# Kernel optimization log

Hardware: AMD Instinct MI355X
Metric: run time of the kernel (lower is better)

The kernel has to match this reference:

```python
import jax, jax.numpy as jnp
import numpy as np

B, S, D = 8, 512, 1024
F = 4 * D        # FFN hidden
E = 8            # num experts
SCALE = 0.02


def setup_inputs() -> dict:
    key = jax.random.key(0)
    ks = jax.random.split(key, 16)
    n = lambda k, shape, s=SCALE: (jax.random.normal(k, shape, dtype=jnp.float32) * s)
    task_ids = jax.random.randint(ks[15], (B,), 0, E)
    return {
        "hidden_states": jax.random.normal(ks[0], (B, S, D), dtype=jnp.float32),
        "ohe_task": jax.nn.one_hot(task_ids, E, dtype=jnp.float32),
        # base model (2-layer FFN) params
        "W1": n(ks[1], (D, F)), "b1": n(ks[2], (F,)),
        "W2": n(ks[3], (F, D)), "b2": n(ks[4], (D,)),
        # expert task vectors (expert_sd - base_sd), stacked over experts
        "T_W1": n(ks[5], (E, D, F)), "T_b1": n(ks[6], (E, F)),
        "T_W2": n(ks[7], (E, F, D)), "T_b2": n(ks[8], (E, D)),
        # gate: 2 hidden ReLU layers then linear to E
        "Wg1": n(ks[9], (D, D)), "bg1": jnp.zeros((D,), jnp.float32),
        "Wg2": n(ks[10], (D, D)), "bg2": jnp.zeros((D,), jnp.float32),
        "Wgo": n(ks[11], (D, E)), "bgo": jnp.zeros((E,), jnp.float32),
    }


def reference(hidden_states, ohe_task, W1, b1, W2, b2,
              T_W1, T_b1, T_W2, T_b2,
              Wg1, bg1, Wg2, bg2, Wgo, bgo):
    x = hidden_states  # [B,S,D]
    # --- router: per-token logits -> softmax over experts -> mean over seq ---
    h = jax.nn.relu(jnp.einsum("bsd,de->bse", x, Wg1) + bg1)
    h = jax.nn.relu(jnp.einsum("bsd,de->bse", h, Wg2) + bg2)
    logits = jnp.einsum("bsd,de->bse", h, Wgo) + bgo        # [B,S,E]
    gate_weights = jax.nn.softmax(logits, axis=-1).mean(axis=1)  # [B,E]
    # --- per-sample weighted merge of expert task vectors into base params ---
    coeff = gate_weights + ohe_task                          # [B,E]
    W1b = W1 + jnp.einsum("be,edf->bdf", coeff, T_W1)        # [B,D,F]
    b1b = b1 + coeff @ T_b1                                  # [B,F]
    W2b = W2 + jnp.einsum("be,efd->bfd", coeff, T_W2)        # [B,F,D]
    b2b = b2 + coeff @ T_b2                                  # [B,D]
    # --- batched functional forward through merged FFN ---
    hmid = jax.nn.gelu(jnp.einsum("bsd,bdf->bsf", x, W1b) + b1b[:, None, :],
                       approximate=False)
    out = jnp.einsum("bsf,bfd->bsd", hmid, W2b) + b2b[:, None, :]
    return out, gate_weights
```

## Files before the change

kernel.cpp:

```cpp
#include <hip/hip_runtime.h>
#include <hip/hip_bf16.h>

typedef __attribute__((ext_vector_type(8))) short s16x8;
typedef __attribute__((ext_vector_type(4))) float f32x4;

#define GLOAD_LDS16(gsrc, ldst) \
  __builtin_amdgcn_global_load_lds((const __attribute__((address_space(1))) void*)(gsrc), \
      (__attribute__((address_space(3))) void*)(ldst), 16, 0, 0)

__global__ __launch_bounds__(256) void cvt_bf16(const float* __restrict__ in,
                                                __hip_bfloat16* __restrict__ out, long n) {
  long i = ((long)blockIdx.x * 256 + threadIdx.x) * 4;
  if (i + 3 >= n) return;
  float4 v = *(const float4*)(in + i);
  __hip_bfloat16 tmp[4] = {__float2bfloat16(v.x), __float2bfloat16(v.y),
                           __float2bfloat16(v.z), __float2bfloat16(v.w)};
  *(ushort4*)((unsigned short*)out + i) = *(const ushort4*)tmp;
}

template<int NB>
__global__ __launch_bounds__(256) void merge_transpose(
    const float* __restrict__ Wb, const float* __restrict__ T,
    const float* __restrict__ coeff, __hip_bfloat16* __restrict__ Out,
    int K, int N, int nE) {
  int ntn = N >> 6;
  int k0 = (blockIdx.x / ntn) << 6;
  int n0 = (blockIdx.x % ntn) << 6;
  int t = threadIdx.x;
  long KN = (long)K * N;

  float4 accb[NB][4];
#pragma unroll
  for (int i = 0; i < 4; ++i) {
    int e = i * 256 + t; int kk = e >> 4, nn = (e & 15) << 2;
    float4 bv = *(const float4*)&Wb[(long)(k0 + kk) * N + n0 + nn];
#pragma unroll
    for (int b2 = 0; b2 < NB; ++b2) accb[b2][i] = bv;
  }
  for (int ex = 0; ex < nE; ++ex) {
    float c[NB];
#pragma unroll
    for (int b2 = 0; b2 < NB; ++b2) c[b2] = coeff[b2 * 8 + ex];
#pragma unroll
    for (int i = 0; i < 4; ++i) {
      int e = i * 256 + t; int kk = e >> 4, nn = (e & 15) << 2;
      float4 tv = *(const float4*)&T[(long)ex * KN + (long)(k0 + kk) * N + n0 + nn];
#pragma unroll
      for (int b2 = 0; b2 < NB; ++b2) {
        accb[b2][i].x += c[b2] * tv.x; accb[b2][i].y += c[b2] * tv.y;
        accb[b2][i].z += c[b2] * tv.z; accb[b2][i].w += c[b2] * tv.w;
      }
    }
  }
  __shared__ __hip_bfloat16 lds[64 * 66];
  for (int b2 = 0; b2 < NB; ++b2) {
    __syncthreads();
#pragma unroll
    for (int i = 0; i < 4; ++i) {
      int e = i * 256 + t; int kk = e >> 4, nn = (e & 15) << 2;
      lds[kk * 66 + nn + 0] = __float2bfloat16(accb[b2][i].x);
      lds[kk * 66 + nn + 1] = __float2bfloat16(accb[b2][i].y);
      lds[kk * 66 + nn + 2] = __float2bfloat16(accb[b2][i].z);
      lds[kk * 66 + nn + 3] = __float2bfloat16(accb[b2][i].w);
    }
    __syncthreads();
#pragma unroll
    for (int i = 0; i < 4; ++i) {
      int o = i * 256 + t; int n2 = o >> 4, k2 = (o & 15) << 2;
      __hip_bfloat16 tmp[4];
#pragma unroll
      for (int j = 0; j < 4; ++j) tmp[j] = lds[(k2 + j) * 66 + n2];
      *(ushort4*)((unsigned short*)&Out[(long)b2 * KN + (long)(n0 + n2) * K + k0 + k2]) =
          *(const ushort4*)tmp;
    }
  }
}

__global__ __launch_bounds__(256) void merge_bias(const float* __restrict__ base,
                                                  const float* __restrict__ T,
                                                  const float* __restrict__ coeff,
                                                  float* __restrict__ out, int n) {
  int b = blockIdx.y;
  int i = blockIdx.x * 256 + threadIdx.x;
  if (i >= n) return;
  float v = base[i];
#pragma unroll
  for (int e = 0; e < 8; ++e) v += coeff[b * 8 + e] * T[(long)e * n + i];
  out[(long)b * n + i] = v;
}

template<int MODE, int ACT, bool OUTBF>
__global__ __launch_bounds__(256, 2) void gemm_bt(
    const __hip_bfloat16* __restrict__ A, const __hip_bfloat16* __restrict__ BT,
    const float* __restrict__ bias, void* __restrict__ Out,
    int N, int K, long sA, long sB, long sBias, long sOut,
    int kLen, long ksOut) {
  int bid = blockIdx.x;
  int b, m, n, kc = 0;
  if (MODE == 0)      { b = blockIdx.y; m = (bid & 7) * 4 + ((bid >> 3) & 3); n = bid >> 5; }
  else                { b = bid & 7; int tile = bid >> 3; m = tile & 3; n = (tile >> 2) & 7; kc = tile >> 5; }
  int m0 = m << 7, n0 = n << 7;
  int kOff = kc * kLen;

  const __hip_bfloat16* Ab = A + (long)b * sA;
  const __hip_bfloat16* Bb = BT + (long)b * sB;

  __shared__ __align__(16) __hip_bfloat16 As[128 * 64];
  __shared__ __align__(16) __hip_bfloat16 Bs[128 * 64];

  int t = threadIdx.x;
  int lane = t & 63;
  int wid = t >> 6;
  int wm = wid >> 1, wn = wid & 1;
  int lr = lane & 15, kg = lane >> 4;

  f32x4 acc[4][4] = {};

  for (int kt = kOff; kt < kOff + kLen; kt += 64) {
#pragma unroll
    for (int is = 0; is < 4; ++is) {
      int ci = is * 256 + t;
      int row = ci >> 3, cpos = ci & 7;
      int csrc = cpos ^ (row & 7);
      GLOAD_LDS16(Ab + (long)(m0 + row) * K + kt + csrc * 8, &As[ci * 8]);
      GLOAD_LDS16(Bb + (long)(n0 + row) * K + kt + csrc * 8, &Bs[ci * 8]);
    }
    __syncthreads();
#pragma unroll
    for (int ks = 0; ks < 2; ++ks) {
      s16x8 af[4], bfr[4];
#pragma unroll
      for (int mi = 0; mi < 4; ++mi) {
        int row = wm * 64 + mi * 16 + lr;
        int c = (ks * 4 + kg) ^ (row & 7);
        af[mi] = *(const s16x8*)&As[row * 64 + c * 8];
      }
#pragma unroll
      for (int ni = 0; ni < 4; ++ni) {
        int row = wn * 64 + ni * 16 + lr;
        int c = (ks * 4 + kg) ^ (row & 7);
        bfr[ni] = *(const s16x8*)&Bs[row * 64 + c * 8];
      }
#pragma unroll
      for (int mi = 0; mi < 4; ++mi)
#pragma unroll
        for (int ni = 0; ni < 4; ++ni)
          acc[mi][ni] = __builtin_amdgcn_mfma_f32_16x16x32_bf16(bfr[ni], af[mi], acc[mi][ni], 0, 0, 0);
    }
    __syncthreads();
  }

#pragma unroll
  for (int mi = 0; mi < 4; ++mi) {
    int row = m0 + wm * 64 + mi * 16 + lr;
#pragma unroll
    for (int ni = 0; ni < 4; ++ni) {
      int colb = n0 + wn * 64 + ni * 16 + kg * 4;
      float bv4[4] = {0.f, 0.f, 0.f, 0.f};
      if (bias != nullptr) {
        float4 bb = *(const float4*)&bias[(long)b * sBias + colb];
        bv4[0] = bb.x; bv4[1] = bb.y; bv4[2] = bb.z; bv4[3] = bb.w;
      }
      float v[4];
#pragma unroll
      for (int j = 0; j < 4; ++j) {
        v[j] = acc[mi][ni][j] + bv4[j];
        if (ACT == 1) v[j] = fmaxf(v[j], 0.f);
        else if (ACT == 2) v[j] = 0.5f * v[j] * (1.f + erff(v[j] * 0.70710678118f));
      }
      long off = kc * ksOut + (long)b * sOut + (long)row * N + colb;
      if (OUTBF) {
        __hip_bfloat16 tmp[4] = {__float2bfloat16(v[0]), __float2bfloat16(v[1]),
                                 __float2bfloat16(v[2]), __float2bfloat16(v[3])};
        *(ushort4*)((unsigned short*)Out + off) = *(const ushort4*)tmp;
      } else {
        *(float4*)((float*)Out + off) = make_float4(v[0], v[1], v[2], v[3]);
      }
    }
  }
}

__global__ __launch_bounds__(512, 4) void gemm_l1(
    const __hip_bfloat16* __restrict__ A, const __hip_bfloat16* __restrict__ BT,
    const float* __restrict__ bias, __hip_bfloat16* __restrict__ Out) {
  const int K = 1024, N = 4096;
  int bid = blockIdx.x;
  int b = bid & 7;
  int tile = bid >> 3;
  int m0 = (tile & 3) << 7;
  int n0 = (tile >> 2) << 8;

  const __hip_bfloat16* Ab = A + (long)b * 512 * 1024;
  const __hip_bfloat16* Bb = BT + (long)b * 4096 * 1024;
  const float* biasb = bias + (long)b * 4096;

  __shared__ __align__(16) __hip_bfloat16 As[128 * 64];
  __shared__ __align__(16) __hip_bfloat16 Bs[256 * 64];

  int t = threadIdx.x;
  int lane = t & 63;
  int wid = t >> 6;
  int wm = wid >> 2;
  int wn = wid & 3;
  int lr = lane & 15, kg = lane >> 4;

  f32x4 acc[4][4] = {};

  for (int kt = 0; kt < K; kt += 64) {
#pragma unroll
    for (int is = 0; is < 2; ++is) {
      int ci = is * 512 + t;
      int row = ci >> 3, cpos = ci & 7;
      int csrc = cpos ^ (row & 7);
      GLOAD_LDS16(Ab + (long)(m0 + row) * K + kt + csrc * 8, &As[ci * 8]);
    }
#pragma unroll
    for (int is = 0; is < 4; ++is) {
      int ci = is * 512 + t;
      int row = ci >> 3, cpos = ci & 7;
      int csrc = cpos ^ (row & 7);
      GLOAD_LDS16(Bb + (long)(n0 + row) * K + kt + csrc * 8, &Bs[ci * 8]);
    }
    __syncthreads();
#pragma unroll
    for (int ks = 0; ks < 2; ++ks) {
      s16x8 af[4], bfr[4];
#pragma unroll
      for (int mi = 0; mi < 4; ++mi) {
        int row = wm * 64 + mi * 16 + lr;
        int c = (ks * 4 + kg) ^ (row & 7);
        af[mi] = *(const s16x8*)&As[row * 64 + c * 8];
      }
#pragma unroll
      for (int ni = 0; ni < 4; ++ni) {
        int row = wn * 64 + ni * 16 + lr;
        int c = (ks * 4 + kg) ^ (row & 7);
        bfr[ni] = *(const s16x8*)&Bs[row * 64 + c * 8];
      }
#pragma unroll
      for (int mi = 0; mi < 4; ++mi)
#pragma unroll
        for (int ni = 0; ni < 4; ++ni)
          acc[mi][ni] = __builtin_amdgcn_mfma_f32_16x16x32_bf16(bfr[ni], af[mi], acc[mi][ni], 0, 0, 0);
    }
    __syncthreads();
  }

#pragma unroll
  for (int mi = 0; mi < 4; ++mi) {
    int row = m0 + wm * 64 + mi * 16 + lr;
#pragma unroll
    for (int ni = 0; ni < 4; ++ni) {
      int colb = n0 + wn * 64 + ni * 16 + kg * 4;
      float4 bb = *(const float4*)&biasb[colb];
      float v[4] = {acc[mi][ni][0] + bb.x, acc[mi][ni][1] + bb.y,
                    acc[mi][ni][2] + bb.z, acc[mi][ni][3] + bb.w};
#pragma unroll
      for (int j = 0; j < 4; ++j)
        v[j] = 0.5f * v[j] * (1.f + erff(v[j] * 0.70710678118f));
      long off = (long)b * 512 * 4096 + (long)row * N + colb;
      __hip_bfloat16 tmp[4] = {__float2bfloat16(v[0]), __float2bfloat16(v[1]),
                               __float2bfloat16(v[2]), __float2bfloat16(v[3])};
      *(ushort4*)((unsigned short*)Out + off) = *(const ushort4*)tmp;
    }
  }
}

__global__ __launch_bounds__(256) void reduce2_bias(
    const __hip_bfloat16* __restrict__ p, const float* __restrict__ b2b,
    float* __restrict__ out, long ksOut) {
  long i = ((long)blockIdx.x * 256 + threadIdx.x) * 8;
  const unsigned short* ps = (const unsigned short*)p;
  ushort4 a0 = *(const ushort4*)(ps + i);
  ushort4 a1 = *(const ushort4*)(ps + i + 4);
  ushort4 c0 = *(const ushort4*)(ps + ksOut + i);
  ushort4 c1 = *(const ushort4*)(ps + ksOut + i + 4);
  int d = (int)(i & 1023);
  int b = (int)(i >> 19);
  const float* bp = b2b + (long)b * 1024 + d;
  float o[8];
  unsigned short av[8] = {a0.x, a0.y, a0.z, a0.w, a1.x, a1.y, a1.z, a1.w};
  unsigned short cv[8] = {c0.x, c0.y, c0.z, c0.w, c1.x, c1.y, c1.z, c1.w};
#pragma unroll
  for (int j = 0; j < 8; ++j) {
    __hip_bfloat16 ab = *(__hip_bfloat16*)&av[j], cb = *(__hip_bfloat16*)&cv[j];
    o[j] = __bfloat162float(ab) + __bfloat162float(cb) + bp[j];
  }
  *(float4*)(out + i) = make_float4(o[0], o[1], o[2], o[3]);
  *(float4*)(out + i + 4) = make_float4(o[4], o[5], o[6], o[7]);
}

__global__ __launch_bounds__(256) void router_logits(
    const __hip_bfloat16* __restrict__ Hg2, const float* __restrict__ Wgo,
    const float* __restrict__ bgo, float* __restrict__ probs) {
  int r = blockIdx.x;
  int t = threadIdx.x;
  float acc[8] = {};
#pragma unroll
  for (int j = 0; j < 4; ++j) {
    int k = j * 256 + t;
    float h = __bfloat162float(Hg2[(long)r * 1024 + k]);
    const float4* wp = (const float4*)&Wgo[k * 8];
    float4 w0 = wp[0], w1 = wp[1];
    acc[0] += h * w0.x; acc[1] += h * w0.y; acc[2] += h * w0.z; acc[3] += h * w0.w;
    acc[4] += h * w1.x; acc[5] += h * w1.y; acc[6] += h * w1.z; acc[7] += h * w1.w;
  }
#pragma unroll
  for (int off = 32; off >= 1; off >>= 1)
#pragma unroll
    for (int e = 0; e < 8; ++e) acc[e] += __shfl_down(acc[e], off);
  __shared__ float lds[4][8];
  int wid = t >> 6, lane = t & 63;
  if (lane == 0)
#pragma unroll
    for (int e = 0; e < 8; ++e) lds[wid][e] = acc[e];
  __syncthreads();
  if (t == 0) {
    float lg[8];
#pragma unroll
    for (int e = 0; e < 8; ++e) lg[e] = lds[0][e] + lds[1][e] + lds[2][e] + lds[3][e] + bgo[e];
    float mx = lg[0];
#pragma unroll
    for (int e = 1; e < 8; ++e) mx = fmaxf(mx, lg[e]);
    float s = 0.f;
#pragma unroll
    for (int e = 0; e < 8; ++e) { lg[e] = __expf(lg[e] - mx); s += lg[e]; }
    float inv = 1.f / s;
#pragma unroll
    for (int e = 0; e < 8; ++e) probs[(long)r * 8 + e] = lg[e] * inv;
  }
}

__global__ __launch_bounds__(256) void router_mean(
    const float* __restrict__ probs, const float* __restrict__ ohe,
    float* __restrict__ gate_out, float* __restrict__ coeff) {
  int b = blockIdx.x;
  int t = threadIdx.x;
  int e = t & 7, sg = t >> 3;
  float s = 0.f;
#pragma unroll
  for (int j = 0; j < 16; ++j)
    s += probs[((long)b * 512 + sg + j * 32) * 8 + e];
  __shared__ float lds[256];
  lds[t] = s;
  __syncthreads();
  if (t < 8) {
    float tot = 0.f;
#pragma unroll
    for (int g = 0; g < 32; ++g) tot += lds[g * 8 + t];
    float gw = tot / 512.f;
    gate_out[b * 8 + t] = gw;
    coeff[b * 8 + t] = gw + ohe[b * 8 + t];
  }
}

extern "C" void kernel_launch(void* const* d_in, const int* in_sizes, int n_in,
                              void* d_out, int out_size, void* d_ws, size_t ws_size,
                              hipStream_t stream) {
  const float* x    = (const float*)d_in[0];
  const float* ohe  = (const float*)d_in[1];
  const float* W1   = (const float*)d_in[2];
  const float* b1   = (const float*)d_in[3];
  const float* W2   = (const float*)d_in[4];
  const float* b2   = (const float*)d_in[5];
  const float* T_W1 = (const float*)d_in[6];
  const float* T_b1 = (const float*)d_in[7];
  const float* T_W2 = (const float*)d_in[8];
  const float* T_b2 = (const float*)d_in[9];
  const float* Wg1  = (const float*)d_in[10];
  const float* bg1  = (const float*)d_in[11];
  const float* Wg2  = (const float*)d_in[12];
  const float* bg2  = (const float*)d_in[13];
  const float* Wgo  = (const float*)d_in[14];
  const float* bgo  = (const float*)d_in[15];
  float* out = (float*)d_out;
  float* gate_out = out + (long)8 * 512 * 1024;

  char* w = (char*)d_ws;
  __hip_bfloat16* xb   = (__hip_bfloat16*)(w);
  __hip_bfloat16* Wg1T = (__hip_bfloat16*)(w + 8388608);
  __hip_bfloat16* Wg2T = (__hip_bfloat16*)(w + 10485760);
  __hip_bfloat16* Hg1  = (__hip_bfloat16*)(w + 12582912);
  __hip_bfloat16* Hg2  = (__hip_bfloat16*)(w + 20971520);
  float*          probs= (float*)(w + 29360128);
  float*          coeff= (float*)(w + 29491200);
  float*          b1b  = (float*)(w + 29492224);
  float*          b2b  = (float*)(w + 29623296);
  __hip_bfloat16* hmid = (__hip_bfloat16*)(w + 29656064);
  __hip_bfloat16* Wb   = (__hip_bfloat16*)(w + 63210496);
  __hip_bfloat16* part = (__hip_bfloat16*)(w);

  const long SSD = (long)512 * 1024;
  const long SSF = (long)512 * 4096;

  cvt_bf16<<<4096, 256, 0, stream>>>(x, xb, (long)8 * 512 * 1024);
  merge_transpose<1><<<16 * 16, 256, 0, stream>>>(Wg1, nullptr, nullptr, Wg1T, 1024, 1024, 0);
  merge_transpose<1><<<16 * 16, 256, 0, stream>>>(Wg2, nullptr, nullptr, Wg2T, 1024, 1024, 0);
  gemm_bt<0, 1, true><<<dim3(256, 1), 256, 0, stream>>>(xb, Wg1T, bg1, Hg1,
      1024, 1024, 0, 0, 0, 0, 1024, 0);
  gemm_bt<0, 1, true><<<dim3(256, 1), 256, 0, stream>>>(Hg1, Wg2T, bg2, Hg2,
      1024, 1024, 0, 0, 0, 0, 1024, 0);
  router_logits<<<4096, 256, 0, stream>>>(Hg2, Wgo, bgo, probs);
  router_mean<<<8, 256, 0, stream>>>(probs, ohe, gate_out, coeff);
  merge_bias<<<dim3(16, 8), 256, 0, stream>>>(b1, T_b1, coeff, b1b, 4096);
  merge_bias<<<dim3(4, 8), 256, 0, stream>>>(b2, T_b2, coeff, b2b, 1024);
  merge_transpose<8><<<16 * 64, 256, 0, stream>>>(W1, T_W1, coeff, Wb, 1024, 4096, 8);
  gemm_l1<<<dim3(512, 1), 512, 0, stream>>>(xb, Wb, b1b, hmid);
  merge_transpose<8><<<64 * 16, 256, 0, stream>>>(W2, T_W2, coeff, Wb, 4096, 1024, 8);
  gemm_bt<2, 0, true><<<dim3(512, 1), 256, 0, stream>>>(hmid, Wb, nullptr, part,
      1024, 4096, SSF, (long)4096 * 1024, 0, SSD, 2048, (long)8 * 512 * 1024);
  reduce2_bias<<<2048, 256, 0, stream>>>(part, b2b, out, (long)8 * 512 * 1024);
}
```

Measured before the change: 258.6 us.

## Fuse layer-1 GEMM with W2 merge in one launch and split K four ways

Adds a combined kernel whose first 512 blocks run the layer-1 GEMM while the remaining 2048 blocks merge and transpose the W2 expert weights into a separate workspace buffer. This overlaps memory-bound merge work with the compute-bound GEMM instead of running them back to back. The second GEMM now uses a 4-way K split (1024 blocks) with a generalized partial-sum reduction, which needs a larger workspace. A fallback path keeps the old sequence when the workspace is too small. The W2 merge blocks use a 64x64 tile with per-element LDS stores, and each block processes 4 of the 8 batches at once.

```diff
diff --git a/kernel.cpp b/kernel.cpp
--- a/kernel.cpp
+++ b/kernel.cpp
@@ -180,11 +180,11 @@
   }
 }
 
-__global__ __launch_bounds__(512, 4) void gemm_l1(
+__device__ __forceinline__ void l1_gemm_body(
+    int bid, int t, __hip_bfloat16* As, __hip_bfloat16* Bs,
     const __hip_bfloat16* __restrict__ A, const __hip_bfloat16* __restrict__ BT,
     const float* __restrict__ bias, __hip_bfloat16* __restrict__ Out) {
   const int K = 1024, N = 4096;
-  int bid = blockIdx.x;
   int b = bid & 7;
   int tile = bid >> 3;
   int m0 = (tile & 3) << 7;
@@ -194,10 +194,6 @@
   const __hip_bfloat16* Bb = BT + (long)b * 4096 * 1024;
   const float* biasb = bias + (long)b * 4096;
 
-  __shared__ __align__(16) __hip_bfloat16 As[128 * 64];
-  __shared__ __align__(16) __hip_bfloat16 Bs[256 * 64];
-
-  int t = threadIdx.x;
   int lane = t & 63;
   int wid = t >> 6;
   int wm = wid >> 2;
@@ -266,25 +262,103 @@
   }
 }
 
-__global__ __launch_bounds__(256) void reduce2_bias(
+__global__ __launch_bounds__(512, 4) void gemm_l1(
+    const __hip_bfloat16* __restrict__ A, const __hip_bfloat16* __restrict__ BT,
+    const float* __restrict__ bias, __hip_bfloat16* __restrict__ Out) {
+  __shared__ __align__(16) __hip_bfloat16 As[128 * 64];
+  __shared__ __align__(16) __hip_bfloat16 Bs[256 * 64];
+  l1_gemm_body(blockIdx.x, threadIdx.x, As, Bs, A, BT, bias, Out);
+}
+
+__global__ __launch_bounds__(512, 4) void fused_l1_w2(
+    const __hip_bfloat16* __restrict__ A, const __hip_bfloat16* __restrict__ BT,
+    const float* __restrict__ bias, __hip_bfloat16* __restrict__ Out,
+    const float* __restrict__ W2, const float* __restrict__ T2,
+    const float* __restrict__ coeff, __hip_bfloat16* __restrict__ Out2) {
+  __shared__ __align__(16) char smem[49152];
+  int bid = blockIdx.x;
+  int t = threadIdx.x;
+  if (bid < 512) {
+    __hip_bfloat16* As = (__hip_bfloat16*)smem;
+    __hip_bfloat16* Bs = As + 128 * 64;
+    l1_gemm_body(bid, t, As, Bs, A, BT, bias, Out);
+    return;
+  }
+  __hip_bfloat16* lds = (__hip_bfloat16*)smem;
+  int mid = bid - 512;
+  int q = (mid & 1) * 4;
+  int tileId = mid >> 1;
+  const int K = 4096, N = 1024;
+  int k0 = (tileId >> 4) << 6;
+  int n0 = (tileId & 15) << 6;
+  long KN = (long)K * N;
+
+  float4 accb[4][2];
+#pragma unroll
+  for (int i = 0; i < 2; ++i) {
+    int c = i * 512 + t; int kk = c >> 4, nn = (c & 15) << 2;
+    float4 bv = *(const float4*)&W2[(long)(k0 + kk) * N + n0 + nn];
+#pragma unroll
+    for (int b2 = 0; b2 < 4; ++b2) accb[b2][i] = bv;
+  }
+  for (int ex = 0; ex < 8; ++ex) {
+    float cf[4];
+#pragma unroll
+    for (int b2 = 0; b2 < 4; ++b2) cf[b2] = coeff[(q + b2) * 8 + ex];
+#pragma unroll
+    for (int i = 0; i < 2; ++i) {
+      int c = i * 512 + t; int kk = c >> 4, nn = (c & 15) << 2;
+      float4 tv = *(const float4*)&T2[(long)ex * KN + (long)(k0 + kk) * N + n0 + nn];
+#pragma unroll
+      for (int b2 = 0; b2 < 4; ++b2) {
+        accb[b2][i].x += cf[b2] * tv.x; accb[b2][i].y += cf[b2] * tv.y;
+        accb[b2][i].z += cf[b2] * tv.z; accb[b2][i].w += cf[b2] * tv.w;
+      }
+    }
+  }
+  for (int b2 = 0; b2 < 4; ++b2) {
+    __syncthreads();
+#pragma unroll
+    for (int i = 0; i < 2; ++i) {
+      int c = i * 512 + t; int kk = c >> 4, nn = (c & 15) << 2;
+      lds[kk * 66 + nn + 0] = __float2bfloat16(accb[b2][i].x);
+      lds[kk * 66 + nn + 1] = __float2bfloat16(accb[b2][i].y);
+      lds[kk * 66 + nn + 2] = __float2bfloat16(accb[b2][i].z);
+      lds[kk * 66 + nn + 3] = __float2bfloat16(accb[b2][i].w);
+    }
+    __syncthreads();
+#pragma unroll
+    for (int i = 0; i < 2; ++i) {
+      int o = i * 512 + t; int n2 = o >> 4, k2 = (o & 15) << 2;
+      __hip_bfloat16 tmp[4];
+#pragma unroll
+      for (int j = 0; j < 4; ++j) tmp[j] = lds[(k2 + j) * 66 + n2];
+      *(ushort4*)((unsigned short*)&Out2[(long)(q + b2) * KN + (long)(n0 + n2) * K + k0 + k2]) =
+          *(const ushort4*)tmp;
+    }
+  }
+}
+
+template<int NP>
+__global__ __launch_bounds__(256) void reduceN_bias(
     const __hip_bfloat16* __restrict__ p, const float* __restrict__ b2b,
     float* __restrict__ out, long ksOut) {
   long i = ((long)blockIdx.x * 256 + threadIdx.x) * 8;
   const unsigned short* ps = (const unsigned short*)p;
-  ushort4 a0 = *(const ushort4*)(ps + i);
-  ushort4 a1 = *(const ushort4*)(ps + i + 4);
-  ushort4 c0 = *(const ushort4*)(ps + ksOut + i);
-  ushort4 c1 = *(const ushort4*)(ps + ksOut + i + 4);
   int d = (int)(i & 1023);
   int b = (int)(i >> 19);
   const float* bp = b2b + (long)b * 1024 + d;
   float o[8];
-  unsigned short av[8] = {a0.x, a0.y, a0.z, a0.w, a1.x, a1.y, a1.z, a1.w};
-  unsigned short cv[8] = {c0.x, c0.y, c0.z, c0.w, c1.x, c1.y, c1.z, c1.w};
-#pragma unroll
-  for (int j = 0; j < 8; ++j) {
-    __hip_bfloat16 ab = *(__hip_bfloat16*)&av[j], cb = *(__hip_bfloat16*)&cv[j];
-    o[j] = __bfloat162float(ab) + __bfloat162float(cb) + bp[j];
+#pragma unroll
+  for (int j = 0; j < 8; ++j) o[j] = bp[j];
+#pragma unroll
+  for (int pp = 0; pp < NP; ++pp) {
+    ushort4 a0 = *(const ushort4*)(ps + pp * ksOut + i);
+    ushort4 a1 = *(const ushort4*)(ps + pp * ksOut + i + 4);
+    unsigned short av[8] = {a0.x, a0.y, a0.z, a0.w, a1.x, a1.y, a1.z, a1.w};
+#pragma unroll
+    for (int j = 0; j < 8; ++j)
+      o[j] += __bfloat162float(*(__hip_bfloat16*)&av[j]);
   }
   *(float4*)(out + i) = make_float4(o[0], o[1], o[2], o[3]);
   *(float4*)(out + i + 4) = make_float4(o[4], o[5], o[6], o[7]);
@@ -388,10 +462,12 @@
   float*          b2b  = (float*)(w + 29623296);
   __hip_bfloat16* hmid = (__hip_bfloat16*)(w + 29656064);
   __hip_bfloat16* Wb   = (__hip_bfloat16*)(w + 63210496);
-  __hip_bfloat16* part = (__hip_bfloat16*)(w);
+  __hip_bfloat16* W2T  = (__hip_bfloat16*)(w + 130319360);
+  bool rich = ws_size >= (size_t)197428224;
 
   const long SSD = (long)512 * 1024;
   const long SSF = (long)512 * 4096;
+  const long OUTN = (long)8 * 512 * 1024;
 
   cvt_bf16<<<4096, 256, 0, stream>>>(x, xb, (long)8 * 512 * 1024);
   merge_transpose<1><<<16 * 16, 256, 0, stream>>>(Wg1, nullptr, nullptr, Wg1T, 1024, 1024, 0);
@@ -405,9 +481,20 @@
   merge_bias<<<dim3(16, 8), 256, 0, stream>>>(b1, T_b1, coeff, b1b, 4096);
   merge_bias<<<dim3(4, 8), 256, 0, stream>>>(b2, T_b2, coeff, b2b, 1024);
   merge_transpose<8><<<16 * 64, 256, 0, stream>>>(W1, T_W1, coeff, Wb, 1024, 4096, 8);
-  gemm_l1<<<dim3(512, 1), 512, 0, stream>>>(xb, Wb, b1b, hmid);
-  merge_transpose<8><<<64 * 16, 256, 0, stream>>>(W2, T_W2, coeff, Wb, 4096, 1024, 8);
-  gemm_bt<2, 0, true><<<dim3(512, 1), 256, 0, stream>>>(hmid, Wb, nullptr, part,
-      1024, 4096, SSF, (long)4096 * 1024, 0, SSD, 2048, (long)8 * 512 * 1024);
-  reduce2_bias<<<2048, 256, 0, stream>>>(part, b2b, out, (long)8 * 512 * 1024);
-}
+
+  if (rich) {
+    fused_l1_w2<<<dim3(2560, 1), 512, 0, stream>>>(xb, Wb, b1b, hmid,
+        W2, T_W2, coeff, W2T);
+    __hip_bfloat16* part = Wb;
+    gemm_bt<2, 0, true><<<dim3(1024, 1), 256, 0, stream>>>(hmid, W2T, nullptr, part,
+        1024, 4096, SSF, (long)4096 * 1024, 0, SSD, 1024, OUTN);
+    reduceN_bias<4><<<2048, 256, 0, stream>>>(part, b2b, out, OUTN);
+  } else {
+    gemm_l1<<<dim3(512, 1), 512, 0, stream>>>(xb, Wb, b1b, hmid);
+    merge_transpose<8><<<64 * 16, 256, 0, stream>>>(W2, T_W2, coeff, Wb, 4096, 1024, 8);
+    __hip_bfloat16* part = xb;
+    gemm_bt<2, 0, true><<<dim3(512, 1), 256, 0, stream>>>(hmid, Wb, nullptr, part,
+        1024, 4096, SSF, (long)4096 * 1024, 0, SSD, 2048, OUTN);
+    reduceN_bias<2><<<2048, 256, 0, stream>>>(part, b2b, out, OUTN);
+  }
+}
```

Result: slower. 292.0 us (+12.9%).

## Generalize 8-wave 128x256 GEMM and use 4-way split-K for second FFN layer

Applied to the files above, without the earlier changes.

Replaces the dedicated first-layer kernel with a templated 8-wave 128x256 tile GEMM that supports split-K, and uses it for the second FFN GEMM too. When the workspace is large enough, the second GEMM is split four ways over K into a separate partial buffer, followed by a 4-way reduction with the bias. This aims to get larger tiles with more reuse while keeping enough blocks to fill the GPU. The trade-off is extra partial-sum traffic in bf16 and a fallback path that depends on workspace size.

```diff
diff --git a/kernel.cpp b/kernel.cpp
--- a/kernel.cpp
+++ b/kernel.cpp
@@ -89,18 +89,15 @@
   out[(long)b * n + i] = v;
 }
 
-template<int MODE, int ACT, bool OUTBF>
+template<int ACT, bool OUTBF>
 __global__ __launch_bounds__(256, 2) void gemm_bt(
     const __hip_bfloat16* __restrict__ A, const __hip_bfloat16* __restrict__ BT,
     const float* __restrict__ bias, void* __restrict__ Out,
-    int N, int K, long sA, long sB, long sBias, long sOut,
-    int kLen, long ksOut) {
+    int N, int K, long sA, long sB, long sBias, long sOut) {
   int bid = blockIdx.x;
-  int b, m, n, kc = 0;
-  if (MODE == 0)      { b = blockIdx.y; m = (bid & 7) * 4 + ((bid >> 3) & 3); n = bid >> 5; }
-  else                { b = bid & 7; int tile = bid >> 3; m = tile & 3; n = (tile >> 2) & 7; kc = tile >> 5; }
+  int b = blockIdx.y;
+  int m = (bid & 7) * 4 + ((bid >> 3) & 3), n = bid >> 5;
   int m0 = m << 7, n0 = n << 7;
-  int kOff = kc * kLen;
 
   const __hip_bfloat16* Ab = A + (long)b * sA;
   const __hip_bfloat16* Bb = BT + (long)b * sB;
@@ -116,13 +113,114 @@
 
   f32x4 acc[4][4] = {};
 
-  for (int kt = kOff; kt < kOff + kLen; kt += 64) {
+  for (int kt = 0; kt < K; kt += 64) {
 #pragma unroll
     for (int is = 0; is < 4; ++is) {
       int ci = is * 256 + t;
       int row = ci >> 3, cpos = ci & 7;
       int csrc = cpos ^ (row & 7);
       GLOAD_LDS16(Ab + (long)(m0 + row) * K + kt + csrc * 8, &As[ci * 8]);
+      GLOAD_LDS16(Bb + (long)(n0 + row) * K + kt + csrc * 8, &Bs[ci * 8]);
+    }
+    __syncthreads();
+#pragma unroll
+    for (int ks = 0; ks < 2; ++ks) {
+      s16x8 af[4], bfr[4];
+#pragma unroll
+      for (int mi = 0; mi < 4; ++mi) {
+        int row = wm * 64 + mi * 16 + lr;
+        int c = (ks * 4 + kg) ^ (row & 7);
+        af[mi] = *(const s16x8*)&As[row * 64 + c * 8];
+      }
+#pragma unroll
+      for (int ni = 0; ni < 4; ++ni) {
+        int row = wn * 64 + ni * 16 + lr;
+        int c = (ks * 4 + kg) ^ (row & 7);
+        bfr[ni] = *(const s16x8*)&Bs[row * 64 + c * 8];
+      }
+#pragma unroll
+      for (int mi = 0; mi < 4; ++mi)
+#pragma unroll
+        for (int ni = 0; ni < 4; ++ni)
+          acc[mi][ni] = __builtin_amdgcn_mfma_f32_16x16x32_bf16(bfr[ni], af[mi], acc[mi][ni], 0, 0, 0);
+    }
+    __syncthreads();
+  }
+
+#pragma unroll
+  for (int mi = 0; mi < 4; ++mi) {
+    int row = m0 + wm * 64 + mi * 16 + lr;
+#pragma unroll
+    for (int ni = 0; ni < 4; ++ni) {
+      int colb = n0 + wn * 64 + ni * 16 + kg * 4;
+      float bv4[4] = {0.f, 0.f, 0.f, 0.f};
+      if (bias != nullptr) {
+        float4 bb = *(const float4*)&bias[(long)b * sBias + colb];
+        bv4[0] = bb.x; bv4[1] = bb.y; bv4[2] = bb.z; bv4[3] = bb.w;
+      }
+      float v[4];
+#pragma unroll
+      for (int j = 0; j < 4; ++j) {
+        v[j] = acc[mi][ni][j] + bv4[j];
+        if (ACT == 1) v[j] = fmaxf(v[j], 0.f);
+        else if (ACT == 2) v[j] = 0.5f * v[j] * (1.f + erff(v[j] * 0.70710678118f));
+      }
+      long off = (long)b * sOut + (long)row * N + colb;
+      if (OUTBF) {
+        __hip_bfloat16 tmp[4] = {__float2bfloat16(v[0]), __float2bfloat16(v[1]),
+                                 __float2bfloat16(v[2]), __float2bfloat16(v[3])};
+        *(ushort4*)((unsigned short*)Out + off) = *(const ushort4*)tmp;
+      } else {
+        *(float4*)((float*)Out + off) = make_float4(v[0], v[1], v[2], v[3]);
+      }
+    }
+  }
+}
+
+template<int ACT, bool OUTBF>
+__global__ __launch_bounds__(512, 4) void gemm8w(
+    const __hip_bfloat16* __restrict__ A, const __hip_bfloat16* __restrict__ BT,
+    const float* __restrict__ bias, void* __restrict__ Out,
+    int N, int K, long sA, long sB, long sBias, long sOut,
+    int kLen, long ksOut, int mBits, int nBits) {
+  int bid = blockIdx.x;
+  int b = bid & 7;
+  int t2 = bid >> 3;
+  int m = t2 & ((1 << mBits) - 1);
+  int rest = t2 >> mBits;
+  int n = rest & ((1 << nBits) - 1);
+  int kc = rest >> nBits;
+  int m0 = m << 7, n0 = n << 8;
+  int kOff = kc * kLen;
+
+  const __hip_bfloat16* Ab = A + (long)b * sA;
+  const __hip_bfloat16* Bb = BT + (long)b * sB;
+
+  __shared__ __align__(16) __hip_bfloat16 As[128 * 64];
+  __shared__ __align__(16) __hip_bfloat16 Bs[256 * 64];
+
+  int t = threadIdx.x;
+  int lane = t & 63;
+  int wid = t >> 6;
+  int wm = wid >> 2;
+  int wn = wid & 3;
+  int lr = lane & 15, kg = lane >> 4;
+
+  f32x4 acc[4][4] = {};
+
+  for (int kt = kOff; kt < kOff + kLen; kt += 64) {
+#pragma unroll
+    for (int is = 0; is < 2; ++is) {
+      int ci = is * 512 + t;
+      int row = ci >> 3, cpos = ci & 7;
+      int csrc = cpos ^ (row & 7);
+      GLOAD_LDS16(Ab + (long)(m0 + row) * K + kt + csrc * 8, &As[ci * 8]);
+    }
+#pragma unroll
+    for (int is = 0; is < 4; ++is) {
+      int ci = is * 512 + t;
+      int row = ci >> 3, cpos = ci & 7;
+      int csrc = cpos ^ (row & 7);
       GLOAD_LDS16(Bb + (long)(n0 + row) * K + kt + csrc * 8, &Bs[ci * 8]);
     }
     __syncthreads();
@@ -180,111 +278,26 @@
   }
 }
 
-__global__ __launch_bounds__(512, 4) void gemm_l1(
-    const __hip_bfloat16* __restrict__ A, const __hip_bfloat16* __restrict__ BT,
-    const float* __restrict__ bias, __hip_bfloat16* __restrict__ Out) {
-  const int K = 1024, N = 4096;
-  int bid = blockIdx.x;
-  int b = bid & 7;
-  int tile = bid >> 3;
-  int m0 = (tile & 3) << 7;
-  int n0 = (tile >> 2) << 8;
-
-  const __hip_bfloat16* Ab = A + (long)b * 512 * 1024;
-  const __hip_bfloat16* Bb = BT + (long)b * 4096 * 1024;
-  const float* biasb = bias + (long)b * 4096;
-
-  __shared__ __align__(16) __hip_bfloat16 As[128 * 64];
-  __shared__ __align__(16) __hip_bfloat16 Bs[256 * 64];
-
-  int t = threadIdx.x;
-  int lane = t & 63;
-  int wid = t >> 6;
-  int wm = wid >> 2;
-  int wn = wid & 3;
-  int lr = lane & 15, kg = lane >> 4;
-
-  f32x4 acc[4][4] = {};
-
-  for (int kt = 0; kt < K; kt += 64) {
-#pragma unroll
-    for (int is = 0; is < 2; ++is) {
-      int ci = is * 512 + t;
-      int row = ci >> 3, cpos = ci & 7;
-      int csrc = cpos ^ (row & 7);
-      GLOAD_LDS16(Ab + (long)(m0 + row) * K + kt + csrc * 8, &As[ci * 8]);
-    }
-#pragma unroll
-    for (int is = 0; is < 4; ++is) {
-      int ci = is * 512 + t;
-      int row = ci >> 3, cpos = ci & 7;
-      int csrc = cpos ^ (row & 7);
-      GLOAD_LDS16(Bb + (long)(n0 + row) * K + kt + csrc * 8, &Bs[ci * 8]);
-    }
-    __syncthreads();
-#pragma unroll
-    for (int ks = 0; ks < 2; ++ks) {
-      s16x8 af[4], bfr[4];
-#pragma unroll
-      for (int mi = 0; mi < 4; ++mi) {
-        int row = wm * 64 + mi * 16 + lr;
-        int c = (ks * 4 + kg) ^ (row & 7);
-        af[mi] = *(const s16x8*)&As[row * 64 + c * 8];
-      }
-#pragma unroll
-      for (int ni = 0; ni < 4; ++ni) {
-        int row = wn * 64 + ni * 16 + lr;
-        int c = (ks * 4 + kg) ^ (row & 7);
-        bfr[ni] = *(const s16x8*)&Bs[row * 64 + c * 8];
-      }
-#pragma unroll
-      for (int mi = 0; mi < 4; ++mi)
-#pragma unroll
-        for (int ni = 0; ni < 4; ++ni)
-          acc[mi][ni] = __builtin_amdgcn_mfma_f32_16x16x32_bf16(bfr[ni], af[mi], acc[mi][ni], 0, 0, 0);
-    }
-    __syncthreads();
-  }
-
-#pragma unroll
-  for (int mi = 0; mi < 4; ++mi) {
-    int row = m0 + wm * 64 + mi * 16 + lr;
-#pragma unroll
-    for (int ni = 0; ni < 4; ++ni) {
-      int colb = n0 + wn * 64 + ni * 16 + kg * 4;
-      float4 bb = *(const float4*)&biasb[colb];
-      float v[4] = {acc[mi][ni][0] + bb.x, acc[mi][ni][1] + bb.y,
-                    acc[mi][ni][2] + bb.z, acc[mi][ni][3] + bb.w};
-#pragma unroll
-      for (int j = 0; j < 4; ++j)
-        v[j] = 0.5f * v[j] * (1.f + erff(v[j] * 0.70710678118f));
-      long off = (long)b * 512 * 4096 + (long)row * N + colb;
-      __hip_bfloat16 tmp[4] = {__float2bfloat16(v[0]), __float2bfloat16(v[1]),
-                               __float2bfloat16(v[2]), __float2bfloat16(v[3])};
-      *(ushort4*)((unsigned short*)Out + off) = *(const ushort4*)tmp;
-    }
-  }
-}
-
-__global__ __launch_bounds__(256) void reduce2_bias(
+template<int NP>
+__global__ __launch_bounds__(256) void reduceN_bias(
     const __hip_bfloat16* __restrict__ p, const float* __restrict__ b2b,
     float* __restrict__ out, long ksOut) {
   long i = ((long)blockIdx.x * 256 + threadIdx.x) * 8;
   const unsigned short* ps = (const unsigned short*)p;
-  ushort4 a0 = *(const ushort4*)(ps + i);
-  ushort4 a1 = *(const ushort4*)(ps + i + 4);
-  ushort4 c0 = *(const ushort4*)(ps + ksOut + i);
-  ushort4 c1 = *(const ushort4*)(ps + ksOut + i + 4);
   int d = (int)(i & 1023);
   int b = (int)(i >> 19);
   const float* bp = b2b + (long)b * 1024 + d;
   float o[8];
-  unsigned short av[8] = {a0.x, a0.y, a0.z, a0.w, a1.x, a1.y, a1.z, a1.w};
-  unsigned short cv[8] = {c0.x, c0.y, c0.z, c0.w, c1.x, c1.y, c1.z, c1.w};
-#pragma unroll
-  for (int j = 0; j < 8; ++j) {
-    __hip_bfloat16 ab = *(__hip_bfloat16*)&av[j], cb = *(__hip_bfloat16*)&cv[j];
-    o[j] = __bfloat162float(ab) + __bfloat162float(cb) + bp[j];
+#pragma unroll
+  for (int j = 0; j < 8; ++j) o[j] = bp[j];
+#pragma unroll
+  for (int pp = 0; pp < NP; ++pp) {
+    ushort4 a0 = *(const ushort4*)(ps + pp * ksOut + i);
+    ushort4 a1 = *(const ushort4*)(ps + pp * ksOut + i + 4);
+    unsigned short av[8] = {a0.x, a0.y, a0.z, a0.w, a1.x, a1.y, a1.z, a1.w};
+#pragma unroll
+    for (int j = 0; j < 8; ++j)
+      o[j] += __bfloat162float(*(__hip_bfloat16*)&av[j]);
   }
   *(float4*)(out + i) = make_float4(o[0], o[1], o[2], o[3]);
   *(float4*)(out + i + 4) = make_float4(o[4], o[5], o[6], o[7]);
@@ -388,26 +401,36 @@
   float*          b2b  = (float*)(w + 29623296);
   __hip_bfloat16* hmid = (__hip_bfloat16*)(w + 29656064);
   __hip_bfloat16* Wb   = (__hip_bfloat16*)(w + 63210496);
-  __hip_bfloat16* part = (__hip_bfloat16*)(w);
+  __hip_bfloat16* partR= (__hip_bfloat16*)(w + 130319360);
+  bool rich = ws_size >= (size_t)197428224;
 
   const long SSD = (long)512 * 1024;
   const long SSF = (long)512 * 4096;
+  const long OUTN = (long)8 * 512 * 1024;
 
   cvt_bf16<<<4096, 256, 0, stream>>>(x, xb, (long)8 * 512 * 1024);
   merge_transpose<1><<<16 * 16, 256, 0, stream>>>(Wg1, nullptr, nullptr, Wg1T, 1024, 1024, 0);
   merge_transpose<1><<<16 * 16, 256, 0, stream>>>(Wg2, nullptr, nullptr, Wg2T, 1024, 1024, 0);
-  gemm_bt<0, 1, true><<<dim3(256, 1), 256, 0, stream>>>(xb, Wg1T, bg1, Hg1,
-      1024, 1024, 0, 0, 0, 0, 1024, 0);
-  gemm_bt<0, 1, true><<<dim3(256, 1), 256, 0, stream>>>(Hg1, Wg2T, bg2, Hg2,
-      1024, 1024, 0, 0, 0, 0, 1024, 0);
+  gemm_bt<1, true><<<dim3(256, 1), 256, 0, stream>>>(xb, Wg1T, bg1, Hg1,
+      1024, 1024, 0, 0, 0, 0);
+  gemm_bt<1, true><<<dim3(256, 1), 256, 0, stream>>>(Hg1, Wg2T, bg2, Hg2,
+      1024, 1024, 0, 0, 0, 0);
   router_logits<<<4096, 256, 0, stream>>>(Hg2, Wgo, bgo, probs);
   router_mean<<<8, 256, 0, stream>>>(probs, ohe, gate_out, coeff);
   merge_bias<<<dim3(16, 8), 256, 0, stream>>>(b1, T_b1, coeff, b1b, 4096);
   merge_bias<<<dim3(4, 8), 256, 0, stream>>>(b2, T_b2, coeff, b2b, 1024);
   merge_transpose<8><<<16 * 64, 256, 0, stream>>>(W1, T_W1, coeff, Wb, 1024, 4096, 8);
-  gemm_l1<<<dim3(512, 1), 512, 0, stream>>>(xb, Wb, b1b, hmid);
+  gemm8w<2, true><<<dim3(512, 1), 512, 0, stream>>>(xb, Wb, b1b, hmid,
+      4096, 1024, SSD, (long)4096 * 1024, 4096, SSF, 1024, 0, 2, 4);
   merge_transpose<8><<<64 * 16, 256, 0, stream>>>(W2, T_W2, coeff, Wb, 4096, 1024, 8);
-  gemm_bt<2, 0, true><<<dim3(512, 1), 256, 0, stream>>>(hmid, Wb, nullptr, part,
-      1024, 4096, SSF, (long)4096 * 1024, 0, SSD, 2048, (long)8 * 512 * 1024);
-  reduce2_bias<<<2048, 256, 0, stream>>>(part, b2b, out, (long)8 * 512 * 1024);
-}
+  if (rich) {
+    gemm8w<0, true><<<dim3(512, 1), 512, 0, stream>>>(hmid, Wb, nullptr, partR,
+        1024, 4096, SSF, (long)4096 * 1024, 0, SSD, 1024, OUTN, 2, 2);
+    reduceN_bias<4><<<2048, 256, 0, stream>>>(partR, b2b, out, OUTN);
+  } else {
+    __hip_bfloat16* part = xb;
+    gemm8w<0, true><<<dim3(256, 1), 512, 0, stream>>>(hmid, Wb, nullptr, part,
+        1024, 4096, SSF, (long)4096 * 1024, 0, SSD, 2048, OUTN, 2, 2);
+    reduceN_bias<2><<<2048, 256, 0, stream>>>(part, b2b, out, OUTN);
+  }
+}
```

After: 260.1 us. No clear change (+0.6%).
